# Performance work log

Hardware: AMD Instinct MI355X
Metric: run time of the kernel (lower is better)

The kernel has to match this reference:

```python
import jax, jax.numpy as jnp
import numpy as np
from jax import lax

# mamba-130m-style config
B, L = 2, 1024          # batch, seq_len
D = 768                 # hidden_size
E = 1536                # intermediate (expand=2)
N = 16                  # ssm state size
R = 48                  # time_step_rank = ceil(D/16)
K = 4                   # conv kernel
NL = 4                  # num layers
NC = 5                  # num classes
EPS = 1e-5


def setup_inputs() -> dict:
    key = jax.random.key(0)
    ks = jax.random.split(key, 10)
    s = 0.02
    return {
        "x": jax.random.normal(ks[0], (B, L, 12), dtype=jnp.float32),
        "proj_w": jax.random.normal(ks[1], (D, 12)) * s,
        "proj_b": jnp.zeros((D,), jnp.float32),
        "norm_w": jnp.ones((NL, D), jnp.float32),
        "in_w": jax.random.normal(ks[2], (NL, 2 * E, D)) * s,
        "conv_w": jax.random.normal(ks[3], (NL, E, K)) * s,
        "conv_b": jnp.zeros((NL, E), jnp.float32),
        "xproj_w": jax.random.normal(ks[4], (NL, R + 2 * N, E)) * s,
        "dt_w": jax.random.normal(ks[5], (NL, E, R)) * s,
        "dt_b": jnp.full((NL, E), -4.0, jnp.float32),  # softplus(-4) ~ small dt
        "A_log": jnp.tile(jnp.log(jnp.arange(1, N + 1, dtype=jnp.float32))[None, None, :], (NL, E, 1)),
        "D_param": jnp.ones((NL, E), jnp.float32),
        "out_w": jax.random.normal(ks[6], (NL, D, E)) * s,
        "fnorm_w": jnp.ones((D,), jnp.float32),
        "cls_w": jax.random.normal(ks[7], (NC, D)) * s,
        "cls_b": jnp.zeros((NC,), jnp.float32),
    }


def _rmsnorm(x, w):
    var = jnp.mean(x * x, axis=-1, keepdims=True)
    return x * lax.rsqrt(var + EPS) * w


def _causal_conv(u, w, b):
    # u: [B,L,E], w: [E,K] depthwise causal conv, left-pad K-1
    up = jnp.pad(u, ((0, 0), (K - 1, 0), (0, 0)))
    y = b
    for k in range(K):
        y = y + w[:, k] * up[:, k:k + L, :]
    return y


def _selective_scan(u, dt, A, Bm, Cm, Dp):
    # u, dt: [B,L,E]; Bm, Cm: [B,L,N]; A: [E,N]; Dp: [E]
    def step(h, inp):
        u_t, dt_t, B_t, C_t = inp  # [B,E],[B,E],[B,N],[B,N]
        dA = jnp.exp(dt_t[:, :, None] * A)                      # [B,E,N]
        h = h * dA + dt_t[:, :, None] * B_t[:, None, :] * u_t[:, :, None]
        y = jnp.einsum('ben,bn->be', h, C_t)
        return h, y

    h0 = jnp.zeros((u.shape[0], E, N), u.dtype)
    _, ys = lax.scan(step, h0,
                     (u.transpose(1, 0, 2), dt.transpose(1, 0, 2),
                      Bm.transpose(1, 0, 2), Cm.transpose(1, 0, 2)))
    return ys.transpose(1, 0, 2) + u * Dp


def reference(x, proj_w, proj_b, norm_w, in_w, conv_w, conv_b, xproj_w,
              dt_w, dt_b, A_log, D_param, out_w, fnorm_w, cls_w, cls_b):
    h = x @ proj_w.T + proj_b                                     # [B,L,D]
    for i in range(NL):
        res = h
        hn = _rmsnorm(h, norm_w[i])
        proj = hn @ in_w[i].T                                     # [B,L,2E]
        u, gate = proj[..., :E], proj[..., E:]
        u = jax.nn.silu(_causal_conv(u, conv_w[i], conv_b[i]))    # [B,L,E]
        xdbc = u @ xproj_w[i].T                                   # [B,L,R+2N]
        dt_r = xdbc[..., :R]
        Bm = xdbc[..., R:R + N]
        Cm = xdbc[..., R + N:]
        dt = jax.nn.softplus(dt_r @ dt_w[i].T + dt_b[i])          # [B,L,E]
        A = -jnp.exp(A_log[i])                                    # [E,N]
        y = _selective_scan(u, dt, A, Bm, Cm, D_param[i])
        y = y * jax.nn.silu(gate)
        h = res + y @ out_w[i].T
    h = _rmsnorm(h, fnorm_w)
    pooled = jnp.mean(h, axis=1)                                  # AdaptiveAvgPool1d(1)
    return pooled @ cls_w.T + cls_b                               # [B,NC]
```

## Files before the change

kernel.cpp:

```cpp
#include <hip/hip_runtime.h>

constexpr int B_  = 2;
constexpr int L_  = 1024;
constexpr int D_  = 768;
constexpr int E_  = 1536;
constexpr int N_  = 16;
constexpr int R_  = 48;
constexpr int NL_ = 4;
constexpr int NC_ = 5;
constexpr int M_  = B_ * L_;
constexpr int E2_ = 2 * E_;
constexpr int XD_ = R_ + 2 * N_;
constexpr float EPS_ = 1e-5f;

constexpr int NCH_ = 16;
constexpr int CL_  = L_ / NCH_;
constexpr int KS_  = 8;
constexpr int XSL_ = E_ / KS_;
constexpr int USTR_ = 200;

typedef __attribute__((ext_vector_type(8))) short bf16x8;
typedef __attribute__((ext_vector_type(4))) float f32x4;
typedef const __attribute__((address_space(1))) void* gas_t;
typedef __attribute__((address_space(3))) void* las_t;

__device__ __forceinline__ float sigm(float x) { return 1.0f / (1.0f + __expf(-x)); }
__device__ __forceinline__ float softplusf(float x) { return x > 20.0f ? x : log1pf(__expf(x)); }
__device__ __forceinline__ ushort f2b(float f) {
  union { float f; unsigned u; } v; v.f = f;
  unsigned r = (v.u + 0x7fffu + ((v.u >> 16) & 1u)) >> 16;
  return (ushort)r;
}
__device__ __forceinline__ float b2f(ushort u) {
  union { unsigned u; float f; } v; v.u = ((unsigned)u) << 16;
  return v.f;
}
__device__ __forceinline__ float b2f_lo(unsigned p) {
  union { unsigned u; float f; } v; v.u = p << 16;
  return v.f;
}
__device__ __forceinline__ float b2f_hi(unsigned p) {
  union { unsigned u; float f; } v; v.u = p & 0xffff0000u;
  return v.f;
}

template <int CTRL>
__device__ __forceinline__ float dpp_add(float x) {
  int yi = __builtin_amdgcn_update_dpp(0, __builtin_bit_cast(int, x), CTRL, 0xf, 0xf, false);
  return x + __builtin_bit_cast(float, yi);
}
__device__ __forceinline__ float row_sum16(float x) {
  x = dpp_add<0x121>(x);
  x = dpp_add<0x122>(x);
  x = dpp_add<0x124>(x);
  x = dpp_add<0x128>(x);
  return x;
}

__device__ __forceinline__ float block_sum(float v, float* sm) {
  #pragma unroll
  for (int o = 32; o > 0; o >>= 1) v += __shfl_xor(v, o);
  if ((threadIdx.x & 63) == 0) sm[threadIdx.x >> 6] = v;
  __syncthreads();
  return sm[0] + sm[1] + sm[2] + sm[3];
}

constexpr int WS1_ = NL_ * E2_ * D_;
constexpr int WS2_ = NL_ * D_ * E_;
constexpr int WS3_ = NL_ * XD_ * E_;
constexpr int WS4_ = NL_ * E_ * 64;
__global__ __launch_bounds__(256) void k_wprep(const float* __restrict__ in_w, const float* __restrict__ out_w,
                                               const float* __restrict__ xw, const float* __restrict__ dw,
                                               ushort* __restrict__ in_wb, ushort* __restrict__ out_wb,
                                               ushort* __restrict__ xwb, ushort* __restrict__ dtwb) {
  int i = (blockIdx.x * 256 + threadIdx.x) * 4;
  if (i < WS1_) {
    float4 v = *(const float4*)(in_w + i);
    *(ushort4*)(in_wb + i) = make_ushort4(f2b(v.x), f2b(v.y), f2b(v.z), f2b(v.w));
  } else if (i < WS1_ + WS2_) {
    int j = i - WS1_;
    float4 v = *(const float4*)(out_w + j);
    *(ushort4*)(out_wb + j) = make_ushort4(f2b(v.x), f2b(v.y), f2b(v.z), f2b(v.w));
  } else if (i < WS1_ + WS2_ + WS3_) {
    int j = i - WS1_ - WS2_;
    float4 v = *(const float4*)(xw + j);
    *(ushort4*)(xwb + j) = make_ushort4(f2b(v.x), f2b(v.y), f2b(v.z), f2b(v.w));
  } else if (i < WS1_ + WS2_ + WS3_ + WS4_) {
    int j = i - WS1_ - WS2_ - WS3_;
    int k = j & 63, e = j >> 6;
    ushort4 o;
    o.x = (k + 0 < R_) ? f2b(dw[e * R_ + k + 0]) : (ushort)0;
    o.y = (k + 1 < R_) ? f2b(dw[e * R_ + k + 1]) : (ushort)0;
    o.z = (k + 2 < R_) ? f2b(dw[e * R_ + k + 2]) : (ushort)0;
    o.w = (k + 3 < R_) ? f2b(dw[e * R_ + k + 3]) : (ushort)0;
    *(ushort4*)(dtwb + j) = o;
  }
}

__global__ __launch_bounds__(256) void k_proj(const float* __restrict__ x, const float* __restrict__ pw,
                                              const float* __restrict__ pb, float* __restrict__ h) {
  __shared__ float xs[12];
  int m = blockIdx.y;
  int d = blockIdx.x * 256 + threadIdx.x;
  if (threadIdx.x < 12) xs[threadIdx.x] = x[m * 12 + threadIdx.x];
  __syncthreads();
  float acc = pb[d];
  #pragma unroll
  for (int j = 0; j < 12; j++) acc = fmaf(xs[j], pw[d * 12 + j], acc);
  h[(size_t)m * D_ + d] = acc;
}

__global__ __launch_bounds__(256) void k_rmsnorm_bf(const float* __restrict__ h, const float* __restrict__ w,
                                                    ushort* __restrict__ hn) {
  __shared__ float sm[4];
  int m = blockIdx.x, tid = threadIdx.x;
  const float* row = h + (size_t)m * D_;
  float v0 = row[tid], v1 = row[tid + 256], v2 = row[tid + 512];
  float s = block_sum(v0 * v0 + v1 * v1 + v2 * v2, sm);
  float sc = rsqrtf(s * (1.0f / D_) + EPS_);
  ushort* o = hn + (size_t)m * D_;
  o[tid]       = f2b(v0 * sc * w[tid]);
  o[tid + 256] = f2b(v1 * sc * w[tid + 256]);
  o[tid + 512] = f2b(v2 * sc * w[tid + 512]);
}

template <int BM, int BN, int MODE>
__global__ __launch_bounds__(256) void k_gemm_bf(const ushort* __restrict__ A, const ushort* __restrict__ Bw,
                                                 void* __restrict__ Cv, const float* __restrict__ res,
                                                 void* __restrict__ Cv2, int Kd, int Nd) {
  constexpr int AM = BM / 32, BNF = BN / 32;
  __shared__ ushort sA[BM * 32];
  __shared__ ushort sB[BN * 32];
  const int tid = threadIdx.x;
  const int wave = tid >> 6, lane = tid & 63;
  const int q = lane >> 4, r = lane & 15;
  const int wm = wave >> 1, wn = wave & 1;
  const int m0 = blockIdx.y * BM, n0 = blockIdx.x * BN;
  f32x4 acc[AM][BNF] = {};

  for (int k0 = 0; k0 < Kd; k0 += 32) {
    #pragma unroll
    for (int j = 0; j < BM / 64; j++) {
      int i = j * 256 + tid;
      const ushort* gp = A + (size_t)(m0 + (i >> 2)) * Kd + k0 + ((i & 3) << 3);
      __builtin_amdgcn_global_load_lds((gas_t)gp, (las_t)(sA + ((j * 256 + wave * 64) << 3)), 16, 0, 0);
    }
    #pragma unroll
    for (int j = 0; j < BN / 64; j++) {
      int i = j * 256 + tid;
      const ushort* gp = Bw + (size_t)(n0 + (i >> 2)) * Kd + k0 + ((i & 3) << 3);
      __builtin_amdgcn_global_load_lds((gas_t)gp, (las_t)(sB + ((j * 256 + wave * 64) << 3)), 16, 0, 0);
    }
    __syncthreads();
    bf16x8 af[AM], bfv[BNF];
    #pragma unroll
    for (int mi = 0; mi < AM; mi++)
      af[mi] = *(const bf16x8*)&sA[(wm * (BM / 2) + mi * 16 + r) * 32 + q * 8];
    #pragma unroll
    for (int nj = 0; nj < BNF; nj++)
      bfv[nj] = *(const bf16x8*)&sB[(wn * (BN / 2) + nj * 16 + r) * 32 + q * 8];
    #pragma unroll
    for (int mi = 0; mi < AM; mi++)
      #pragma unroll
      for (int nj = 0; nj < BNF; nj++)
        acc[mi][nj] = __builtin_amdgcn_mfma_f32_16x16x32_bf16(af[mi], bfv[nj], acc[mi][nj], 0, 0, 0);
    __syncthreads();
  }
  #pragma unroll
  for (int mi = 0; mi < AM; mi++) {
    #pragma unroll
    for (int nj = 0; nj < BNF; nj++) {
      int col = n0 + wn * (BN / 2) + nj * 16 + r;
      #pragma unroll
      for (int rg = 0; rg < 4; rg++) {
        int row = m0 + wm * (BM / 2) + mi * 16 + q * 4 + rg;
        float v = acc[mi][nj][rg];
        if (MODE == 4) {
          if (col >= E_) {
            v = v * sigm(v);
            ((ushort*)Cv2)[(size_t)row * E_ + col - E_] = f2b(v);
          } else {
            ((ushort*)Cv)[(size_t)row * E_ + col] = f2b(v);
          }
        } else if (MODE == 6) {
          ((ushort*)Cv)[(size_t)row * Nd + col] = f2b(softplusf(v + res[col]));
        } else {
          size_t off = (size_t)row * Nd + col;
          if (MODE == 1) v += res[off];
          ((float*)Cv)[off] = v;
        }
      }
    }
  }
}

__global__ __launch_bounds__(256) void k_gemm_xc(const ushort* __restrict__ proju, const float* __restrict__ cw,
                                                 const float* __restrict__ cb, const ushort* __restrict__ Bw,
                                                 ushort* __restrict__ ub16, float* __restrict__ part) {
  __shared__ ushort sU[64 * USTR_];
  __shared__ ushort sB[80 * USTR_];
  const int tid = threadIdx.x;
  const int wave = tid >> 6, lane = tid & 63;
  const int q = lane >> 4, r = lane & 15;
  const int m0 = blockIdx.x * 64;
  const int kbeg = blockIdx.y * XSL_;

  for (int i = tid; i < 80 * (XSL_ / 8); i += 256) {
    int row = i / (XSL_ / 8), seg = i % (XSL_ / 8);
    bf16x8 v = *(const bf16x8*)(Bw + (size_t)row * E_ + kbeg + seg * 8);
    *(bf16x8*)&sB[row * USTR_ + seg * 8] = v;
  }

  for (int i = tid; i < 64 * (XSL_ / 4); i += 256) {
    int row = i / (XSL_ / 4), e4i = i % (XSL_ / 4);
    int e = kbeg + e4i * 4;
    int m = m0 + row;
    int t = m & (L_ - 1);
    float4 w0 = *(const float4*)(cw + (e + 0) * 4);
    float4 w1 = *(const float4*)(cw + (e + 1) * 4);
    float4 w2 = *(const float4*)(cw + (e + 2) * 4);
    float4 w3 = *(const float4*)(cw + (e + 3) * 4);
    float wv[4][4] = {{w0.x, w0.y, w0.z, w0.w}, {w1.x, w1.y, w1.z, w1.w},
                      {w2.x, w2.y, w2.z, w2.w}, {w3.x, w3.y, w3.z, w3.w}};
    float4 bb = *(const float4*)(cb + e);
    float acc[4] = {bb.x, bb.y, bb.z, bb.w};
    #pragma unroll
    for (int k = 0; k < 4; k++) {
      int tt = t + k - 3;
      if (tt >= 0) {
        uint2 p = *(const uint2*)(proju + (size_t)(m + k - 3) * E_ + e);
        acc[0] = fmaf(wv[0][k], b2f_lo(p.x), acc[0]);
        acc[1] = fmaf(wv[1][k], b2f_hi(p.x), acc[1]);
        acc[2] = fmaf(wv[2][k], b2f_lo(p.y), acc[2]);
        acc[3] = fmaf(wv[3][k], b2f_hi(p.y), acc[3]);
      }
    }
    float u0 = acc[0] * sigm(acc[0]), u1 = acc[1] * sigm(acc[1]);
    float u2 = acc[2] * sigm(acc[2]), u3 = acc[3] * sigm(acc[3]);
    uint2 uo;
    uo.x = (unsigned)f2b(u0) | ((unsigned)f2b(u1) << 16);
    uo.y = (unsigned)f2b(u2) | ((unsigned)f2b(u3) << 16);
    *(uint2*)(ub16 + (size_t)m * E_ + e) = uo;
    *(uint2*)&sU[row * USTR_ + e4i * 4] = uo;
  }
  __syncthreads();

  f32x4 acc[5] = {};
  #pragma unroll
  for (int k0 = 0; k0 < XSL_ / 32; k0++) {
    bf16x8 af = *(const bf16x8*)&sU[(wave * 16 + r) * USTR_ + k0 * 32 + q * 8];
    #pragma unroll
    for (int nj = 0; nj < 5; nj++) {
      bf16x8 bfv = *(const bf16x8*)&sB[(nj * 16 + r) * USTR_ + k0 * 32 + q * 8];
      acc[nj] = __builtin_amdgcn_mfma_f32_16x16x32_bf16(af, bfv, acc[nj], 0, 0, 0);
    }
  }
  float* pp = part + (size_t)blockIdx.y * M_ * XD_;
  #pragma unroll
  for (int nj = 0; nj < 5; nj++) {
    int col = nj * 16 + r;
    #pragma unroll
    for (int rg = 0; rg < 4; rg++) {
      int row = m0 + wave * 16 + q * 4 + rg;
      pp[(size_t)row * XD_ + col] = acc[nj][rg];
    }
  }
}

__global__ __launch_bounds__(256) void k_xfin(const float* __restrict__ part, float* __restrict__ xdbc,
                                              ushort* __restrict__ xb) {
  int i = blockIdx.x * 256 + threadIdx.x;
  int m = i / XD_, col = i - m * XD_;
  float s = 0.0f;
  #pragma unroll
  for (int ks = 0; ks < KS_; ks++) s += part[(size_t)ks * M_ * XD_ + i];
  xdbc[i] = s;
  if (col < R_) xb[(size_t)m * 64 + col] = f2b(s);
  else if (col < 64) xb[(size_t)m * 64 + col] = 0;
}

__global__ __launch_bounds__(256, 6) void k_scanA(const ushort* __restrict__ u, const ushort* __restrict__ dtb,
                                                  const float* __restrict__ xdbc, const float* __restrict__ A_log,
                                                  float* __restrict__ Pst, float* __restrict__ Sst) {
  __shared__ float2 s_dtu[CL_][16];
  __shared__ float  s_b [CL_][16];
  const int tid = threadIdx.x;
  const int e0 = blockIdx.x << 4;
  const int b  = blockIdx.y;
  const int c  = blockIdx.z;
  const int n  = tid & 15, el = tid >> 4;
  const int e  = e0 + el;
  const float A = -__expf(A_log[e * N_ + n]);
  const int t0 = c * CL_;

  ushort r_dt[4], r_u[4];
  float r_b[4];
  #pragma unroll
  for (int j = 0; j < 4; j++) {
    size_t m = (size_t)(b * L_ + t0 + j * 16 + el);
    r_dt[j] = dtb[m * E_ + e0 + n];
    r_u[j]  = u[m * E_ + e0 + n];
    int idx = j * 256 + tid;
    r_b[j] = xdbc[(size_t)(b * L_ + t0 + (idx >> 4)) * XD_ + R_ + (idx & 15)];
  }
  #pragma unroll
  for (int j = 0; j < 4; j++) {
    int t = j * 16 + el;
    float dtv = b2f(r_dt[j]);
    s_dtu[t][n] = make_float2(dtv, dtv * b2f(r_u[j]));
    int idx = j * 256 + tid;
    s_b[idx >> 4][idx & 15] = r_b[j];
  }
  __syncthreads();

  float hs = 0.0f, pp = 1.0f;
  #pragma unroll 8
  for (int t = 0; t < CL_; t++) {
    float2 dtu = s_dtu[t][el];
    float dA = __expf(dtu.x * A);
    hs = fmaf(hs, dA, dtu.y * s_b[t][n]);
    pp *= dA;
  }
  size_t o = (((size_t)(b * NCH_ + c) * E_) + e) * N_ + n;
  Pst[o] = pp;
  Sst[o] = hs;
}

__global__ __launch_bounds__(256, 6) void k_scanC(const ushort* __restrict__ u, const ushort* __restrict__ dtb,
                                                  const float* __restrict__ xdbc, const ushort* __restrict__ gb,
                                                  const float* __restrict__ A_log, const float* __restrict__ Dp,
                                                  const float* __restrict__ Pst, const float* __restrict__ Sst,
                                                  ushort* __restrict__ y) {
  __shared__ float2 s_dtu[CL_][16];
  __shared__ float2 s_bc [CL_][16];
  __shared__ float2 s_og [CL_][16];
  __shared__ ushort s_y [CL_][16];
  const int tid = threadIdx.x;
  const int e0 = blockIdx.x << 4;
  const int b  = blockIdx.y;
  const int c  = blockIdx.z;
  const int n  = tid & 15, el = tid >> 4;
  const int e  = e0 + el;
  const float A = -__expf(A_log[e * N_ + n]);
  const float Dv = Dp[e0 + n];
  const int t0 = c * CL_;

  ushort r_dt[4], r_u[4], r_g[4];
  float r_bc[8];
  #pragma unroll
  for (int j = 0; j < 4; j++) {
    size_t m = (size_t)(b * L_ + t0 + j * 16 + el);
    r_dt[j] = dtb[m * E_ + e0 + n];
    r_u[j]  = u[m * E_ + e0 + n];
    r_g[j]  = gb[m * E_ + e0 + n];
  }
  #pragma unroll
  for (int j = 0; j < 8; j++) {
    int idx = j * 256 + tid;
    r_bc[j] = xdbc[(size_t)(b * L_ + t0 + (idx >> 5)) * XD_ + R_ + (idx & 31)];
  }

  float hs = 0.0f;
  if (c > 0) {
    float pv[NCH_ - 1], sv[NCH_ - 1];
    #pragma unroll
    for (int cc = 0; cc < NCH_ - 1; cc++) {
      int ci = cc < c ? cc : c - 1;
      size_t o = (((size_t)(b * NCH_ + ci) * E_) + e) * N_ + n;
      pv[cc] = Pst[o];
      sv[cc] = Sst[o];
    }
    #pragma unroll
    for (int cc = 0; cc < NCH_ - 1; cc++) {
      bool v = cc < c;
      hs = fmaf(v ? pv[cc] : 1.0f, hs, v ? sv[cc] : 0.0f);
    }
  }

  #pragma unroll
  for (int j = 0; j < 4; j++) {
    int t = j * 16 + el;
    float dtv = b2f(r_dt[j]);
    float uf = b2f(r_u[j]);
    s_dtu[t][n] = make_float2(dtv, dtv * uf);
    s_og[t][n] = make_float2(uf * Dv, b2f(r_g[j]));
  }
  #pragma unroll
  for (int j = 0; j < 8; j++) {
    int idx = j * 256 + tid;
    int t = idx >> 5, col = idx & 31;
    ((float*)&s_bc[t][0])[((col & 15) << 1) + (col >> 4)] = r_bc[j];
  }
  __syncthreads();

  #pragma unroll 8
  for (int t = 0; t < CL_; t++) {
    float2 dtu = s_dtu[t][el];
    float2 bc  = s_bc[t][n];
    float dA = __expf(dtu.x * A);
    hs = fmaf(hs, dA, dtu.y * bc.x);
    float p = row_sum16(hs * bc.y);
    if (n == 0) {
      float2 og = s_og[t][el];
      s_y[t][el] = f2b((p + og.x) * og.y);
    }
  }
  __syncthreads();

  {
    int row = tid >> 2, seg = tid & 3;
    uint2 v = *(const uint2*)&s_y[row][seg * 4];
    *(uint2*)(y + (size_t)(b * L_ + t0 + row) * E_ + e0 + seg * 4) = v;
  }
}

__global__ __launch_bounds__(256) void k_rowscale(const float* __restrict__ h, float* __restrict__ rs) {
  __shared__ float sm[4];
  int m = blockIdx.x, tid = threadIdx.x;
  const float* row = h + (size_t)m * D_;
  float v0 = row[tid], v1 = row[tid + 256], v2 = row[tid + 512];
  float s = block_sum(v0 * v0 + v1 * v1 + v2 * v2, sm);
  if (tid == 0) rs[m] = rsqrtf(s * (1.0f / D_) + EPS_);
}

__global__ __launch_bounds__(256) void k_pool(const float* __restrict__ h, const float* __restrict__ rs,
                                              const float* __restrict__ fw, float* __restrict__ pooled) {
  int d = blockIdx.x * 256 + threadIdx.x;
  int t0 = blockIdx.y * 128;
  int b = blockIdx.z;
  float acc = 0.0f;
  for (int t = t0; t < t0 + 128; t++) {
    int m = b * L_ + t;
    acc = fmaf(h[(size_t)m * D_ + d], rs[m], acc);
  }
  atomicAdd(&pooled[b * D_ + d], acc * fw[d] * (1.0f / L_));
}

__global__ __launch_bounds__(256) void k_logits(const float* __restrict__ pooled, const float* __restrict__ cw,
                                                const float* __restrict__ cb, float* __restrict__ out) {
  int wv = threadIdx.x >> 6, ln = threadIdx.x & 63;
  for (int p = wv; p < B_ * NC_; p += 4) {
    int b = p / NC_, c = p % NC_;
    float s = 0.0f;
    for (int d = ln; d < D_; d += 64) s = fmaf(pooled[b * D_ + d], cw[c * D_ + d], s);
    #pragma unroll
    for (int o = 32; o > 0; o >>= 1) s += __shfl_xor(s, o);
    if (ln == 0) out[p] = s + cb[c];
  }
}

extern "C" void kernel_launch(void* const* d_in, const int* in_sizes, int n_in,
                              void* d_out, int out_size, void* d_ws, size_t ws_size,
                              hipStream_t stream) {
  const float* x       = (const float*)d_in[0];
  const float* proj_w  = (const float*)d_in[1];
  const float* proj_b  = (const float*)d_in[2];
  const float* norm_w  = (const float*)d_in[3];
  const float* in_w    = (const float*)d_in[4];
  const float* conv_w  = (const float*)d_in[5];
  const float* conv_b  = (const float*)d_in[6];
  const float* xproj_w = (const float*)d_in[7];
  const float* dt_w    = (const float*)d_in[8];
  const float* dt_b    = (const float*)d_in[9];
  const float* A_log   = (const float*)d_in[10];
  const float* D_param = (const float*)d_in[11];
  const float* out_w   = (const float*)d_in[12];
  const float* fnorm_w = (const float*)d_in[13];
  const float* cls_w   = (const float*)d_in[14];
  const float* cls_b   = (const float*)d_in[15];
  float* out = (float*)d_out;

  float* h      = (float*)d_ws;
  float* xdbc   = h + (size_t)M_ * D_;
  float* rsb    = xdbc + (size_t)M_ * XD_;
  float* pooled = rsb + M_;
  float* Pst    = pooled + B_ * D_;
  float* Sst    = Pst + (size_t)B_ * NCH_ * E_ * N_;
  float* xpart  = Sst + (size_t)B_ * NCH_ * E_ * N_;
  ushort* proju_bf = (ushort*)(xpart + (size_t)KS_ * M_ * XD_);
  ushort* g_bf    = proju_bf + (size_t)M_ * E_;
  ushort* hn_bf   = g_bf + (size_t)M_ * E_;
  ushort* y_bf    = hn_bf + (size_t)M_ * D_;
  ushort* ub_bf   = y_bf + (size_t)M_ * E_;
  ushort* dt_bf   = ub_bf + (size_t)M_ * E_;
  ushort* xdbc_bf = dt_bf + (size_t)M_ * E_;
  ushort* xwb     = xdbc_bf + (size_t)M_ * 64;
  ushort* dtwb    = xwb + (size_t)NL_ * XD_ * E_;
  ushort* in_wb   = dtwb + (size_t)NL_ * E_ * 64;
  ushort* out_wb  = in_wb + (size_t)NL_ * E2_ * D_;

  constexpr int WTOT = WS1_ + WS2_ + WS3_ + WS4_;
  k_wprep<<<(WTOT / 4 + 255) / 256, 256, 0, stream>>>(in_w, out_w, xproj_w, dt_w,
                                                      in_wb, out_wb, xwb, dtwb);

  k_proj<<<dim3(D_ / 256, M_), 256, 0, stream>>>(x, proj_w, proj_b, h);

  for (int i = 0; i < NL_; i++) {
    k_rmsnorm_bf<<<M_, 256, 0, stream>>>(h, norm_w + i * D_, hn_bf);
    k_gemm_bf<64, 128, 4><<<dim3(E2_ / 128, M_ / 64), 256, 0, stream>>>(
        hn_bf, in_wb + (size_t)i * E2_ * D_, proju_bf, nullptr, g_bf, D_, E2_);
    k_gemm_xc<<<dim3(M_ / 64, KS_), 256, 0, stream>>>(proju_bf, conv_w + i * E_ * 4, conv_b + i * E_,
                                                      xwb + (size_t)i * XD_ * E_, ub_bf, xpart);
    k_xfin<<<M_ * XD_ / 256, 256, 0, stream>>>(xpart, xdbc, xdbc_bf);
    k_gemm_bf<64, 64, 6><<<dim3(E_ / 64, M_ / 64), 256, 0, stream>>>(
        xdbc_bf, dtwb + (size_t)i * E_ * 64, dt_bf, dt_b + i * E_, nullptr, 64, E_);
    k_scanA<<<dim3(E_ / 16, B_, NCH_), 256, 0, stream>>>(ub_bf, dt_bf, xdbc,
                                                         A_log + (size_t)i * E_ * N_, Pst, Sst);
    k_scanC<<<dim3(E_ / 16, B_, NCH_), 256, 0, stream>>>(ub_bf, dt_bf, xdbc, g_bf,
                                                         A_log + (size_t)i * E_ * N_, D_param + i * E_,
                                                         Pst, Sst, y_bf);
    k_gemm_bf<64, 64, 1><<<dim3(D_ / 64, M_ / 64), 256, 0, stream>>>(
        y_bf, out_wb + (size_t)i * D_ * E_, h, h, nullptr, E_, D_);
  }

  k_rowscale<<<M_, 256, 0, stream>>>(h, rsb);
  hipMemsetAsync(pooled, 0, (size_t)B_ * D_ * sizeof(float), stream);
  k_pool<<<dim3(D_ / 256, L_ / 128, B_), 256, 0, stream>>>(h, rsb, fnorm_w, pooled);
  k_logits<<<1, 256, 0, stream>>>(pooled, cls_w, cls_b, out);
}
```

Baseline: 707.9 us.

## Fuse split-K reduction into xproj GEMM via last-block counter; enlarge in-proj tile

Removes the separate k_xfin launch: each split-K block of the x-projection GEMM increments a per-row-block atomic counter, and the last arriving block reduces all partials and writes xdbc and its bf16 copy. Counters are zeroed inside the weight-prep kernel. The in-projection GEMM moves to a 128x128 tile, and the final pooling drops its memset and atomics in favour of one block per (d-slice, batch) looping over all of L. This trades launch overhead for a serialized tail reduction, less parallelism in pooling, and fewer blocks in the in-projection GEMM.

Result: slower. 846.9 us (+19.6%).

```diff
diff --git a/kernel.cpp b/kernel.cpp
--- a/kernel.cpp
+++ b/kernel.cpp
@@ -18,6 +18,7 @@
 constexpr int KS_  = 8;
 constexpr int XSL_ = E_ / KS_;
 constexpr int USTR_ = 200;
+constexpr int NMB_ = M_ / 64;
 
 typedef __attribute__((ext_vector_type(8))) short bf16x8;
 typedef __attribute__((ext_vector_type(4))) float f32x4;
@@ -72,7 +73,9 @@
 __global__ __launch_bounds__(256) void k_wprep(const float* __restrict__ in_w, const float* __restrict__ out_w,
                                                const float* __restrict__ xw, const float* __restrict__ dw,
                                                ushort* __restrict__ in_wb, ushort* __restrict__ out_wb,
-                                               ushort* __restrict__ xwb, ushort* __restrict__ dtwb) {
+                                               ushort* __restrict__ xwb, ushort* __restrict__ dtwb,
+                                               int* __restrict__ cnt) {
+  if (blockIdx.x == 0 && threadIdx.x < NL_ * NMB_) cnt[threadIdx.x] = 0;
   int i = (blockIdx.x * 256 + threadIdx.x) * 4;
   if (i < WS1_) {
     float4 v = *(const float4*)(in_w + i);
@@ -196,7 +199,9 @@
 
 __global__ __launch_bounds__(256) void k_gemm_xc(const ushort* __restrict__ proju, const float* __restrict__ cw,
                                                  const float* __restrict__ cb, const ushort* __restrict__ Bw,
-                                                 ushort* __restrict__ ub16, float* __restrict__ part) {
+                                                 ushort* __restrict__ ub16, float* __restrict__ part,
+                                                 int* __restrict__ cnt, float* __restrict__ xdbc,
+                                                 ushort* __restrict__ xb) {
   __shared__ ushort sU[64 * USTR_];
   __shared__ ushort sB[80 * USTR_];
   const int tid = threadIdx.x;
@@ -265,18 +270,29 @@
       pp[(size_t)row * XD_ + col] = acc[nj][rg];
     }
   }
-}
-
-__global__ __launch_bounds__(256) void k_xfin(const float* __restrict__ part, float* __restrict__ xdbc,
-                                              ushort* __restrict__ xb) {
-  int i = blockIdx.x * 256 + threadIdx.x;
-  int m = i / XD_, col = i - m * XD_;
-  float s = 0.0f;
-  #pragma unroll
-  for (int ks = 0; ks < KS_; ks++) s += part[(size_t)ks * M_ * XD_ + i];
-  xdbc[i] = s;
-  if (col < R_) xb[(size_t)m * 64 + col] = f2b(s);
-  else if (col < 64) xb[(size_t)m * 64 + col] = 0;
+
+  __syncthreads();
+  __shared__ int s_last;
+  if (tid == 0) {
+    __threadfence();
+    s_last = atomicAdd(cnt + blockIdx.x, 1);
+  }
+  __syncthreads();
+  if (s_last == KS_ - 1) {
+    __threadfence();
+    for (int i = tid; i < 64 * XD_; i += 256) {
+      int row = m0 + i / XD_, col = i % XD_;
+      float s = 0.0f;
+      #pragma unroll
+      for (int ks = 0; ks < KS_; ks++) s += part[(size_t)ks * M_ * XD_ + (size_t)row * XD_ + col];
+      xdbc[(size_t)row * XD_ + col] = s;
+      if (col < R_) xb[(size_t)row * 64 + col] = f2b(s);
+    }
+    for (int i = tid; i < 64 * 16; i += 256) {
+      int row = m0 + (i >> 4);
+      xb[(size_t)row * 64 + R_ + (i & 15)] = 0;
+    }
+  }
 }
 
 __global__ __launch_bounds__(256, 6) void k_scanA(const ushort* __restrict__ u, const ushort* __restrict__ dtb,
@@ -426,14 +442,13 @@
 __global__ __launch_bounds__(256) void k_pool(const float* __restrict__ h, const float* __restrict__ rs,
                                               const float* __restrict__ fw, float* __restrict__ pooled) {
   int d = blockIdx.x * 256 + threadIdx.x;
-  int t0 = blockIdx.y * 128;
-  int b = blockIdx.z;
+  int b = blockIdx.y;
   float acc = 0.0f;
-  for (int t = t0; t < t0 + 128; t++) {
+  for (int t = 0; t < L_; t++) {
     int m = b * L_ + t;
     acc = fmaf(h[(size_t)m * D_ + d], rs[m], acc);
   }
-  atomicAdd(&pooled[b * D_ + d], acc * fw[d] * (1.0f / L_));
+  pooled[b * D_ + d] = acc * fw[d] * (1.0f / L_);
 }
 
 __global__ __launch_bounds__(256) void k_logits(const float* __restrict__ pooled, const float* __restrict__ cw,
@@ -477,7 +492,8 @@
   float* Pst    = pooled + B_ * D_;
   float* Sst    = Pst + (size_t)B_ * NCH_ * E_ * N_;
   float* xpart  = Sst + (size_t)B_ * NCH_ * E_ * N_;
-  ushort* proju_bf = (ushort*)(xpart + (size_t)KS_ * M_ * XD_);
+  int*   cnt    = (int*)(xpart + (size_t)KS_ * M_ * XD_);
+  ushort* proju_bf = (ushort*)(cnt + NL_ * NMB_);
   ushort* g_bf    = proju_bf + (size_t)M_ * E_;
   ushort* hn_bf   = g_bf + (size_t)M_ * E_;
   ushort* y_bf    = hn_bf + (size_t)M_ * D_;
@@ -491,17 +507,17 @@
 
   constexpr int WTOT = WS1_ + WS2_ + WS3_ + WS4_;
   k_wprep<<<(WTOT / 4 + 255) / 256, 256, 0, stream>>>(in_w, out_w, xproj_w, dt_w,
-                                                      in_wb, out_wb, xwb, dtwb);
+                                                      in_wb, out_wb, xwb, dtwb, cnt);
 
   k_proj<<<dim3(D_ / 256, M_), 256, 0, stream>>>(x, proj_w, proj_b, h);
 
   for (int i = 0; i < NL_; i++) {
     k_rmsnorm_bf<<<M_, 256, 0, stream>>>(h, norm_w + i * D_, hn_bf);
-    k_gemm_bf<64, 128, 4><<<dim3(E2_ / 128, M_ / 64), 256, 0, stream>>>(
+    k_gemm_bf<128, 128, 4><<<dim3(E2_ / 128, M_ / 128), 256, 0, stream>>>(
         hn_bf, in_wb + (size_t)i * E2_ * D_, proju_bf, nullptr, g_bf, D_, E2_);
     k_gemm_xc<<<dim3(M_ / 64, KS_), 256, 0, stream>>>(proju_bf, conv_w + i * E_ * 4, conv_b + i * E_,
-                                                      xwb + (size_t)i * XD_ * E_, ub_bf, xpart);
-    k_xfin<<<M_ * XD_ / 256, 256, 0, stream>>>(xpart, xdbc, xdbc_bf);
+                                                      xwb + (size_t)i * XD_ * E_, ub_bf, xpart,
+                                                      cnt + i * NMB_, xdbc, xdbc_bf);
     k_gemm_bf<64, 64, 6><<<dim3(E_ / 64, M_ / 64), 256, 0, stream>>>(
         xdbc_bf, dtwb + (size_t)i * E_ * 64, dt_bf, dt_b + i * E_, nullptr, 64, E_);
     k_scanA<<<dim3(E_ / 16, B_, NCH_), 256, 0, stream>>>(ub_bf, dt_bf, xdbc,
@@ -514,7 +530,6 @@
   }
 
   k_rowscale<<<M_, 256, 0, stream>>>(h, rsb);
-  hipMemsetAsync(pooled, 0, (size_t)B_ * D_ * sizeof(float), stream);
-  k_pool<<<dim3(D_ / 256, L_ / 128, B_), 256, 0, stream>>>(h, rsb, fnorm_w, pooled);
+  k_pool<<<dim3(D_ / 256, B_), 256, 0, stream>>>(h, rsb, fnorm_w, pooled);
   k_logits<<<1, 256, 0, stream>>>(pooled, cls_w, cls_b, out);
 }
```
